# Optimization experiments

Measured on AMD Instinct MI355X. Metric: run time of the kernel, lower is better.

The kernel has to match this reference:

```python
import jax, jax.numpy as jnp
import numpy as np

N = 100000       # num nodes
E = 1600000      # num edges
D_IN = 32
D_HID = 32
D_OUT = 32
K = 3            # Chebyshev order (number of terms)


def setup_inputs() -> dict:
    key = jax.random.key(0)
    k1, k2, k3, k4, k5, k6 = jax.random.split(key, 6)
    x = jax.random.normal(k1, (N, D_IN), dtype=jnp.float32)
    edge_index = jax.random.randint(k2, (2, E), 0, N, dtype=jnp.int64)
    s1 = 1.0 / np.sqrt(D_IN)
    s2 = 1.0 / np.sqrt(D_HID)
    W1 = jax.random.uniform(k3, (K, D_IN, D_HID), jnp.float32, -s1, s1)
    b1 = jax.random.uniform(k4, (D_HID,), jnp.float32, -s1, s1)
    W2 = jax.random.uniform(k5, (K, D_HID, D_OUT), jnp.float32, -s2, s2)
    b2 = jax.random.uniform(k6, (D_OUT,), jnp.float32, -s2, s2)
    return {"x": x, "edge_index": edge_index, "W1": W1, "b1": b1, "W2": W2, "b2": b2}


def _prop(x, row, col, w):
    # L_hat @ x : gather along col, scale by edge weight, scatter-add to row.
    # (diagonal of the rescaled Laplacian cancels to 0 in PyG ChebConv with
    #  sym normalization and lambda_max=2, so only off-diagonal edges remain)
    return jax.ops.segment_sum(w[:, None] * x[col], row, num_segments=N)


def _cheb_conv(x, row, col, w, W, b):
    # Chebyshev recurrence: Tx0 = x, Tx1 = L_hat x, Tx_k = 2 L_hat Tx_{k-1} - Tx_{k-2}
    k_terms = W.shape[0]
    Tx0 = x
    out = Tx0 @ W[0]
    if k_terms > 1:
        Tx1 = _prop(Tx0, row, col, w)
        out = out + Tx1 @ W[1]
        for k in range(2, k_terms):
            Tx2 = 2.0 * _prop(Tx1, row, col, w) - Tx0
            out = out + Tx2 @ W[k]
            Tx0, Tx1 = Tx1, Tx2
    return out + b


def reference(x, edge_index, W1, b1, W2, b2):
    row, col = edge_index[0], edge_index[1]
    mask = (row != col).astype(x.dtype)            # remove_self_loops
    deg = jax.ops.segment_sum(mask, row, num_segments=N)
    dinv = jnp.where(deg > 0, 1.0 / jnp.sqrt(jnp.maximum(deg, 1.0)), 0.0)
    w = -mask * dinv[row] * dinv[col]              # scaled Laplacian off-diagonal weights
    x0 = x
    h = jax.nn.relu(_cheb_conv(x, row, col, w, W1, b1))
    h = _cheb_conv(h, row, col, w, W2, b2)
    return h + x0
```

## Files before the change

kernel.cpp:

```cpp
#include <hip/hip_runtime.h>

#define NN 100000
#define EE 1600000
#define DD 32
#define NBUK 196
#define BROWS 512
#define TILE 4096
#define NT 391
#define BCAP2 10240
#define BSLOT 12288

typedef unsigned int uint;
typedef unsigned short ushort;
typedef unsigned char uchar;
typedef __attribute__((ext_vector_type(8))) short bf16x8;
typedef __attribute__((ext_vector_type(4))) float f32x4;

__device__ __forceinline__ ushort f2b(float f) {
    uint u = __float_as_uint(f);
    u += 0x7fffu + ((u >> 16) & 1u);
    return (ushort)(u >> 16);
}
__device__ __forceinline__ float b2f(ushort h) {
    return __uint_as_float((uint)h << 16);
}
__device__ __forceinline__ uint f2e4(float f) {
    uint u = __float_as_uint(f);
    uint s = (u >> 24) & 0x80u;
    float a = fabsf(f) * 0x1p-120f;
    uint g = __float_as_uint(a);
    g += 0x7FFFFu + ((g >> 20) & 1u);
    uint m = g >> 20;
    if (m > 0x7Eu) m = 0x7Eu;
    return s | m;
}
__device__ __forceinline__ bf16x8 as_bf16x8(uint4 v) {
    union { uint4 u; bf16x8 b; } cv; cv.u = v; return cv.b;
}
__device__ __forceinline__ void acc8(float* acc, uint2 v) {
#pragma unroll
    for (int wi = 0; wi < 2; ++wi) {
        uint w = (&v.x)[wi];
        acc[wi * 4 + 0] += 0x1p120f * __uint_as_float(((w & 0x80u) << 24) | ((w & 0x7fu) << 20));
        acc[wi * 4 + 1] += 0x1p120f * __uint_as_float(((w & 0x8000u) << 16) | ((w & 0x7f00u) << 12));
        acc[wi * 4 + 2] += 0x1p120f * __uint_as_float(((w & 0x800000u) << 8) | ((w & 0x7f0000u) << 4));
        acc[wi * 4 + 3] += 0x1p120f * __uint_as_float((w & 0x80000000u) | ((w & 0x7f000000u) >> 4));
    }
}


__global__ void k_part(const int* __restrict__ ei, int* __restrict__ gtail,
                       int* __restrict__ pairs) {
    __shared__ int hist[256];
    __shared__ int gbase[256];
    int t = threadIdx.x;
    hist[t] = 0;
    __syncthreads();
    int e0 = blockIdx.x * TILE;
    int pk[16], rk[16], bb[16];
#pragma unroll
    for (int k = 0; k < 16; ++k) {
        int e = e0 + t + k * 256;
        bb[k] = -1;
        if (e < EE) {
            int r = ei[e], c = ei[EE + e];
            if (r != c) {
                bb[k] = r >> 9;
                pk[k] = (r & (BROWS - 1)) | (c << 9);
                rk[k] = atomicAdd(&hist[bb[k]], 1);
            }
        }
    }
    __syncthreads();
    if (t < NBUK) {
        int cnt = hist[t];
        gbase[t] = cnt ? atomicAdd(&gtail[t * 16], cnt) : 0;
    }
    __syncthreads();
#pragma unroll
    for (int k = 0; k < 16; ++k) {
        if (bb[k] >= 0) {
            int pos = gbase[bb[k]] + rk[k];
            if (pos < BCAP2) pairs[bb[k] * BCAP2 + pos] = pk[k];
        }
    }
}


__global__ void k_build2(const int* __restrict__ gtail, const int* __restrict__ pairs,
                         float* __restrict__ dinv, int* __restrict__ desc,
                         int* __restrict__ ghist, int* __restrict__ ent) {
    __shared__ int lcnt[BROWS];
    __shared__ int loff[BROWS];
    __shared__ int part[256];
    __shared__ int lh[16];
    __shared__ int slab[BSLOT];
    int b = blockIdx.x, t = threadIdx.x;
    lcnt[t] = 0; lcnt[t + 256] = 0;
    if (t < 16) lh[t] = 0;
    __syncthreads();
    int cnt = gtail[b * 16]; if (cnt > BCAP2) cnt = BCAP2;
    const int* pp = pairs + b * BCAP2;
    for (int i = t; i < cnt; i += 256)
        atomicAdd(&lcnt[pp[i] & (BROWS - 1)], 1);
    __syncthreads();
    int v0 = lcnt[2 * t], v1 = lcnt[2 * t + 1];
    int s0 = v0 > 64 ? 64 : v0; s0 = (s0 + 7) & ~7;
    int s1 = v1 > 64 ? 64 : v1; s1 = (s1 + 7) & ~7;
    part[t] = s0 + s1;
    __syncthreads();
    for (int d = 1; d < 256; d <<= 1) {
        int x = part[t];
        int y = (t >= d) ? part[t - d] : 0;
        __syncthreads();
        part[t] = x + y;
        __syncthreads();
    }
    int excl = (t == 0) ? 0 : part[t - 1];
    loff[2 * t] = excl;
    loff[2 * t + 1] = excl + s0;
    __syncthreads();
    int rowbase = b * BROWS;
    for (int lr = t; lr < BROWS; lr += 256) {
        int n = rowbase + lr;
        if (n < NN) {
            int d = lcnt[lr];
            int ms = d > 64 ? 64 : d;
            int cls = (ms + 7) >> 3;
            dinv[n] = d > 0 ? rsqrtf((float)d) : 0.0f;
            desc[n] = ((b * BSLOT + loff[lr]) >> 3) | (cls << 24);
            atomicAdd(&lh[cls], 1);
        }
    }
    __syncthreads();
    if (t < 16 && lh[t]) atomicAdd(&ghist[t], lh[t]);
    lcnt[t] = 0; lcnt[t + 256] = 0;
    for (int i = t; i < BSLOT; i += 256) slab[i] = NN;
    __syncthreads();
    for (int i = t; i < cnt; i += 256) {
        int v = pp[i];
        int lr = v & (BROWS - 1);
        int pos = atomicAdd(&lcnt[lr], 1);
        if (pos < 64) slab[loff[lr] + pos] = (int)((uint)v >> 9);
    }
    __syncthreads();
    int padded = part[255];
    for (int i = t; i < padded; i += 256)
        ent[(size_t)b * BSLOT + i] = slab[i];
}


__global__ void k_perms(const int* __restrict__ desc, int* __restrict__ classcur,
                        int2* __restrict__ pdesc) {
    __shared__ int h[16];
    __shared__ int base[16];
    if (threadIdx.x < 16) h[threadIdx.x] = 0;
    __syncthreads();
    int n = blockIdx.x * blockDim.x + threadIdx.x;
    int d = 0, cls = 0, rk = 0;
    if (n < NN) {
        d = desc[n];
        cls = (d >> 24) & 15;
        rk = atomicAdd(&h[cls], 1);
    }
    __syncthreads();
    if (threadIdx.x < 16 && h[threadIdx.x])
        base[threadIdx.x] = atomicAdd(&classcur[threadIdx.x], h[threadIdx.x]);
    __syncthreads();
    if (n < NN) {
        int2 v; v.x = n; v.y = d;
        pdesc[base[cls] + rk] = v;
    }
}


__global__ void k_cvt(const float* __restrict__ x, uint2* __restrict__ xb,
                      uint* __restrict__ xb8, const float* __restrict__ dinv,
                      const float* __restrict__ W1, const float* __restrict__ W2,
                      ushort* __restrict__ wb1, ushort* __restrict__ wb2,
                      const int* __restrict__ ghist, int* __restrict__ classcur,
                      uint* __restrict__ t1b8, uint* __restrict__ hb8) {
    if (blockIdx.x == (NN * DD / 4) / 256) {
        for (int i = threadIdx.x; i < 6144; i += 256) {
            const float* W = W1; ushort* wb = wb1;
            int ii = i;
            if (ii >= 3072) { ii -= 3072; W = W2; wb = wb2; }
            int term = ii >> 10, rem = ii & 1023;
            int h = rem >> 9, lane = (rem >> 3) & 63, j = rem & 7;
            int k = ((lane >> 4) << 3) + j;
            int col = (h << 4) | (lane & 15);
            wb[ii] = f2b(W[term * 1024 + k * 32 + col]);
        }
        return;
    }
    if (blockIdx.x == 0) {
        if (threadIdx.x == 0) {
            int s = 0;
            for (int i = 0; i < 16; ++i) { classcur[i] = s; s += ghist[i]; }
        }
        if (threadIdx.x >= 64 && threadIdx.x < 72) xb8[NN * 8 + threadIdx.x - 64] = 0;
        if (threadIdx.x >= 72 && threadIdx.x < 80) t1b8[NN * 8 + threadIdx.x - 72] = 0;
        if (threadIdx.x >= 80 && threadIdx.x < 88) hb8[NN * 8 + threadIdx.x - 80] = 0;
    }
    int tid = blockIdx.x * blockDim.x + threadIdx.x;
    if (tid >= NN * DD / 4) return;
    float4 v = ((const float4*)x)[tid];
    uint2 b;
    b.x = (uint)f2b(v.x) | ((uint)f2b(v.y) << 16);
    b.y = (uint)f2b(v.z) | ((uint)f2b(v.w) << 16);
    xb[tid] = b;
    float dv = dinv[tid >> 3];
    xb8[tid] = f2e4(dv * v.x) | (f2e4(dv * v.y) << 8)
             | (f2e4(dv * v.z) << 16) | (f2e4(dv * v.w) << 24);
}


__global__ void k_prop(const int2* __restrict__ pdesc, const int* __restrict__ ent,
                       const float* __restrict__ dinv,
                       const uint2* __restrict__ src8d,
                       const uint4* __restrict__ baseq,
                       uint2* __restrict__ dst8d,
                       uint4* __restrict__ dstbq,
                       float alpha, float beta) {
    int tid = blockIdx.x * blockDim.x + threadIdx.x;
    int g = tid >> 3;
    if (g >= NN) return;
    int sub = tid & 3, h = (tid >> 2) & 1;
    int2 pd = pdesc[g];
    int n = pd.x;
    const int* ep = ent + ((size_t)(pd.y & 0xFFFFFF) << 3);
    int mr = ((pd.y >> 24) & 15) << 3;
    float acc[8] = {0, 0, 0, 0, 0, 0, 0, 0};
    for (int i = h * 8; i < mr; i += 16) {
        uint4 C0 = *(const uint4*)(ep + i);
        uint4 C1 = *(const uint4*)(ep + i + 4);
        uint2 v0 = src8d[(C0.x << 2) + sub];
        uint2 v1 = src8d[(C0.y << 2) + sub];
        uint2 v2 = src8d[(C0.z << 2) + sub];
        uint2 v3 = src8d[(C0.w << 2) + sub];
        uint2 v4 = src8d[(C1.x << 2) + sub];
        uint2 v5 = src8d[(C1.y << 2) + sub];
        uint2 v6 = src8d[(C1.z << 2) + sub];
        uint2 v7 = src8d[(C1.w << 2) + sub];
        acc8(acc, v0);
        acc8(acc, v1);
        acc8(acc, v2);
        acc8(acc, v3);
        acc8(acc, v4);
        acc8(acc, v5);
        acc8(acc, v6);
        acc8(acc, v7);
    }
    float dn = dinv[n];
    float s = -alpha * dn;
#pragma unroll
    for (int k = 0; k < 8; ++k)
        acc[k] = s * (acc[k] + __shfl_xor(acc[k], 4, 64));
    if (baseq) {
        uint4 b = baseq[(n << 2) + sub];
#pragma unroll
        for (int wi = 0; wi < 4; ++wi) {
            uint w = (&b.x)[wi];
            acc[wi * 2 + 0] += beta * __uint_as_float(w << 16);
            acc[wi * 2 + 1] += beta * __uint_as_float(w & 0xffff0000u);
        }
    }
    if (h == 0) {
        uint4 ob;
#pragma unroll
        for (int wi = 0; wi < 4; ++wi)
            (&ob.x)[wi] = (uint)f2b(acc[wi * 2]) | ((uint)f2b(acc[wi * 2 + 1]) << 16);
        dstbq[(n << 2) + sub] = ob;
    } else if (dst8d) {
        uint2 o8;
        o8.x = f2e4(dn * acc[0]) | (f2e4(dn * acc[1]) << 8)
             | (f2e4(dn * acc[2]) << 16) | (f2e4(dn * acc[3]) << 24);
        o8.y = f2e4(dn * acc[4]) | (f2e4(dn * acc[5]) << 8)
             | (f2e4(dn * acc[6]) << 16) | (f2e4(dn * acc[7]) << 24);
        dst8d[(n << 2) + sub] = o8;
    }
}


__global__ void k_comb(const uint4* __restrict__ t0, const uint4* __restrict__ t1,
                       const uint4* __restrict__ t2, const ushort* __restrict__ wb,
                       const float* __restrict__ bias, const float* __restrict__ residf,
                       const float* __restrict__ dinv,
                       float* __restrict__ outf, ushort* __restrict__ outb,
                       uchar* __restrict__ outb8, int do_relu) {
    int lane = threadIdx.x & 63;
    int wid = threadIdx.x >> 6;
    int n0 = (blockIdx.x * 4 + wid) << 6;
    if (n0 >= NN) return;
    int q = lane >> 4, lr = lane & 15;
    const uint4* wq = (const uint4*)wb;
    bf16x8 bf[3][2];
#pragma unroll
    for (int t = 0; t < 3; ++t)
#pragma unroll
        for (int h = 0; h < 2; ++h)
            bf[t][h] = as_bf16x8(wq[((t * 2 + h) << 6) + lane]);
    float bias0 = bias[lr], bias1 = bias[16 + lr];
    uint4 z; z.x = 0; z.y = 0; z.z = 0; z.w = 0;
#pragma unroll
    for (int mt = 0; mt < 4; ++mt) {
        int nb = n0 + (mt << 4);
        int row = nb + lr;
        bool ok = row < NN;
        int ai = (row << 2) + q;
        bf16x8 a0 = as_bf16x8(ok ? t0[ai] : z);
        bf16x8 a1 = as_bf16x8(ok ? t1[ai] : z);
        bf16x8 a2 = as_bf16x8(ok ? t2[ai] : z);
        f32x4 c0 = {0.f, 0.f, 0.f, 0.f};
        f32x4 c1 = {0.f, 0.f, 0.f, 0.f};
        c0 = __builtin_amdgcn_mfma_f32_16x16x32_bf16(a0, bf[0][0], c0, 0, 0, 0);
        c0 = __builtin_amdgcn_mfma_f32_16x16x32_bf16(a1, bf[1][0], c0, 0, 0, 0);
        c0 = __builtin_amdgcn_mfma_f32_16x16x32_bf16(a2, bf[2][0], c0, 0, 0, 0);
        c1 = __builtin_amdgcn_mfma_f32_16x16x32_bf16(a0, bf[0][1], c1, 0, 0, 0);
        c1 = __builtin_amdgcn_mfma_f32_16x16x32_bf16(a1, bf[1][1], c1, 0, 0, 0);
        c1 = __builtin_amdgcn_mfma_f32_16x16x32_bf16(a2, bf[2][1], c1, 0, 0, 0);
#pragma unroll
        for (int r = 0; r < 4; ++r) {
            int node = nb + (q << 2) + r;
            if (node >= NN) continue;
            float v0 = c0[r] + bias0;
            float v1 = c1[r] + bias1;
            if (do_relu) { v0 = fmaxf(v0, 0.0f); v1 = fmaxf(v1, 0.0f); }
            if (outb) {
                float dv = dinv[node];
                outb[node * DD + lr] = f2b(v0);
                outb[node * DD + 16 + lr] = f2b(v1);
                outb8[node * DD + lr] = (uchar)f2e4(dv * v0);
                outb8[node * DD + 16 + lr] = (uchar)f2e4(dv * v1);
            } else {
                outf[node * DD + lr] = v0 + residf[node * DD + lr];
                outf[node * DD + 16 + lr] = v1 + residf[node * DD + 16 + lr];
            }
        }
    }
}


extern "C" void kernel_launch(void* const* d_in, const int* in_sizes, int n_in,
                              void* d_out, int out_size, void* d_ws, size_t ws_size,
                              hipStream_t stream) {
    const float* x  = (const float*)d_in[0];
    const int*   ei = (const int*)d_in[1];
    const float* W1 = (const float*)d_in[2];
    const float* b1 = (const float*)d_in[3];
    const float* W2 = (const float*)d_in[4];
    const float* b2 = (const float*)d_in[5];
    float* out = (float*)d_out;

    char* wsp = (char*)d_ws;
    size_t off = 0;
    auto take = [&](size_t bytes) {
        char* p = wsp + off;
        off = (off + bytes + 255) & ~(size_t)255;
        return p;
    };
    int*    ctrl  = (int*)take((size_t)(NBUK * 16 + 32) * 4);
    int*    gtail = ctrl;
    int*    ghist = ctrl + NBUK * 16;
    int*    ccur  = ctrl + NBUK * 16 + 16;
    float*  dinv  = (float*)take((size_t)NN * 4);
    int*    desc  = (int*)take((size_t)NN * 4);
    int2*   pdesc = (int2*)take((size_t)NN * 8);
    ushort* wb1   = (ushort*)take((size_t)3072 * 2);
    ushort* wb2   = (ushort*)take((size_t)3072 * 2);
    int*    pairs = (int*)take((size_t)NBUK * BCAP2 * 4);
    int*    ent   = (int*)take((size_t)NBUK * BSLOT * 4);
    ushort* xb    = (ushort*)take((size_t)NN * DD * 2);
    ushort* t1b   = (ushort*)take((size_t)NN * DD * 2);
    ushort* t2b   = (ushort*)take((size_t)NN * DD * 2);
    ushort* hb    = (ushort*)take((size_t)NN * DD * 2);
    uchar*  xb8   = (uchar*)take((size_t)(NN + 1) * DD);
    uchar*  t1b8  = (uchar*)take((size_t)(NN + 1) * DD);
    uchar*  hb8   = (uchar*)take((size_t)(NN + 1) * DD);

    hipMemsetAsync(ctrl, 0, (size_t)(NBUK * 16 + 32) * 4, stream);

    k_part  <<<NT, 256, 0, stream>>>(ei, gtail, pairs);
    k_build2<<<NBUK, 256, 0, stream>>>(gtail, pairs, dinv, desc, ghist, ent);
    k_cvt   <<<NN * DD / 4 / 256 + 1, 256, 0, stream>>>(x, (uint2*)xb, (uint*)xb8, dinv,
                                                        W1, W2, wb1, wb2, ghist, ccur,
                                                        (uint*)t1b8, (uint*)hb8);
    k_perms <<<(NN + 255) / 256, 256, 0, stream>>>(desc, ccur, pdesc);

    const int pgrid = (NN * 8 + 255) / 256;
    const int mgrid = (NN + 255) / 256;
    k_prop<<<pgrid, 256, 0, stream>>>(pdesc, ent, dinv, (const uint2*)xb8, nullptr,
                                      (uint2*)t1b8, (uint4*)t1b, 1.0f, 0.0f);
    k_prop<<<pgrid, 256, 0, stream>>>(pdesc, ent, dinv, (const uint2*)t1b8,
                                      (const uint4*)xb, nullptr, (uint4*)t2b, 2.0f, -1.0f);
    k_comb<<<mgrid, 256, 0, stream>>>((const uint4*)xb, (const uint4*)t1b,
                                      (const uint4*)t2b, wb1, b1, nullptr, dinv,
                                      nullptr, hb, hb8, 1);
    k_prop<<<pgrid, 256, 0, stream>>>(pdesc, ent, dinv, (const uint2*)hb8, nullptr,
                                      (uint2*)t1b8, (uint4*)t1b, 1.0f, 0.0f);
    k_prop<<<pgrid, 256, 0, stream>>>(pdesc, ent, dinv, (const uint2*)t1b8,
                                      (const uint4*)hb, nullptr, (uint4*)t2b, 2.0f, -1.0f);
    k_comb<<<mgrid, 256, 0, stream>>>((const uint4*)hb, (const uint4*)t1b,
                                      (const uint4*)t2b, wb2, b2, x, dinv,
                                      out, nullptr, nullptr, 0);
}
```

Baseline: 255.4 us.

## Halve bucket size, fold class prefix into build and perms into convert kernel

Buckets now cover 256 rows instead of 512, giving 391 smaller buckets so the build kernel runs more blocks with one row per thread and less shared memory. The class-offset prefix sum moves into the last-finishing build block, found with a done counter and threadfence. The permutation kernel is merged into the convert kernel as extra blocks, removing one launch. This relies on last-block detection being correct, and smaller bucket capacities raise the risk of overflow and silently dropped edges.

```diff
diff --git a/kernel.cpp b/kernel.cpp
--- a/kernel.cpp
+++ b/kernel.cpp
@@ -3,12 +3,13 @@
 #define NN 100000
 #define EE 1600000
 #define DD 32
-#define NBUK 196
-#define BROWS 512
+#define NBUK 391
+#define BROWS 256
 #define TILE 4096
 #define NT 391
-#define BCAP2 10240
-#define BSLOT 12288
+#define BCAP2 4864
+#define BSLOT 5888
+#define CVB 3125
 
 typedef unsigned int uint;
 typedef unsigned short ushort;
@@ -51,10 +52,10 @@
 
 __global__ void k_part(const int* __restrict__ ei, int* __restrict__ gtail,
                        int* __restrict__ pairs) {
-    __shared__ int hist[256];
-    __shared__ int gbase[256];
+    __shared__ int hist[512];
+    __shared__ int gbase[512];
     int t = threadIdx.x;
-    hist[t] = 0;
+    hist[t] = 0; hist[t + 256] = 0;
     __syncthreads();
     int e0 = blockIdx.x * TILE;
     int pk[16], rk[16], bb[16];
@@ -65,16 +66,16 @@
         if (e < EE) {
             int r = ei[e], c = ei[EE + e];
             if (r != c) {
-                bb[k] = r >> 9;
-                pk[k] = (r & (BROWS - 1)) | (c << 9);
+                bb[k] = r >> 8;
+                pk[k] = (r & (BROWS - 1)) | (c << 8);
                 rk[k] = atomicAdd(&hist[bb[k]], 1);
             }
         }
     }
     __syncthreads();
-    if (t < NBUK) {
-        int cnt = hist[t];
-        gbase[t] = cnt ? atomicAdd(&gtail[t * 16], cnt) : 0;
+    for (int q = t; q < NBUK; q += 256) {
+        int cnt = hist[q];
+        gbase[q] = cnt ? atomicAdd(&gtail[q * 16], cnt) : 0;
     }
     __syncthreads();
 #pragma unroll
@@ -89,14 +90,16 @@
 
 __global__ void k_build2(const int* __restrict__ gtail, const int* __restrict__ pairs,
                          float* __restrict__ dinv, int* __restrict__ desc,
-                         int* __restrict__ ghist, int* __restrict__ ent) {
+                         int* __restrict__ ghist, int* __restrict__ ent,
+                         int* __restrict__ done, int* __restrict__ classcur) {
     __shared__ int lcnt[BROWS];
     __shared__ int loff[BROWS];
     __shared__ int part[256];
     __shared__ int lh[16];
     __shared__ int slab[BSLOT];
+    __shared__ int isLast;
     int b = blockIdx.x, t = threadIdx.x;
-    lcnt[t] = 0; lcnt[t + 256] = 0;
+    lcnt[t] = 0;
     if (t < 16) lh[t] = 0;
     __syncthreads();
     int cnt = gtail[b * 16]; if (cnt > BCAP2) cnt = BCAP2;
@@ -104,10 +107,9 @@
     for (int i = t; i < cnt; i += 256)
         atomicAdd(&lcnt[pp[i] & (BROWS - 1)], 1);
     __syncthreads();
-    int v0 = lcnt[2 * t], v1 = lcnt[2 * t + 1];
+    int v0 = lcnt[t];
     int s0 = v0 > 64 ? 64 : v0; s0 = (s0 + 7) & ~7;
-    int s1 = v1 > 64 ? 64 : v1; s1 = (s1 + 7) & ~7;
-    part[t] = s0 + s1;
+    part[t] = s0;
     __syncthreads();
     for (int d = 1; d < 256; d <<= 1) {
         int x = part[t];
@@ -116,60 +118,42 @@
         part[t] = x + y;
         __syncthreads();
     }
-    int excl = (t == 0) ? 0 : part[t - 1];
-    loff[2 * t] = excl;
-    loff[2 * t + 1] = excl + s0;
-    __syncthreads();
-    int rowbase = b * BROWS;
-    for (int lr = t; lr < BROWS; lr += 256) {
-        int n = rowbase + lr;
-        if (n < NN) {
-            int d = lcnt[lr];
-            int ms = d > 64 ? 64 : d;
-            int cls = (ms + 7) >> 3;
-            dinv[n] = d > 0 ? rsqrtf((float)d) : 0.0f;
-            desc[n] = ((b * BSLOT + loff[lr]) >> 3) | (cls << 24);
-            atomicAdd(&lh[cls], 1);
-        }
+    int excl = part[t] - s0;
+    loff[t] = excl;
+    int n = b * BROWS + t;
+    if (n < NN) {
+        int d = v0;
+        int ms = d > 64 ? 64 : d;
+        int cls = (ms + 7) >> 3;
+        dinv[n] = d > 0 ? rsqrtf((float)d) : 0.0f;
+        desc[n] = ((b * BSLOT + excl) >> 3) | (cls << 24);
+        atomicAdd(&lh[cls], 1);
     }
     __syncthreads();
     if (t < 16 && lh[t]) atomicAdd(&ghist[t], lh[t]);
-    lcnt[t] = 0; lcnt[t + 256] = 0;
+    lcnt[t] = 0;
     for (int i = t; i < BSLOT; i += 256) slab[i] = NN;
     __syncthreads();
     for (int i = t; i < cnt; i += 256) {
         int v = pp[i];
         int lr = v & (BROWS - 1);
         int pos = atomicAdd(&lcnt[lr], 1);
-        if (pos < 64) slab[loff[lr] + pos] = (int)((uint)v >> 9);
+        if (pos < 64) slab[loff[lr] + pos] = (int)((uint)v >> 8);
     }
     __syncthreads();
     int padded = part[255];
     for (int i = t; i < padded; i += 256)
         ent[(size_t)b * BSLOT + i] = slab[i];
-}
-
-
-__global__ void k_perms(const int* __restrict__ desc, int* __restrict__ classcur,
-                        int2* __restrict__ pdesc) {
-    __shared__ int h[16];
-    __shared__ int base[16];
-    if (threadIdx.x < 16) h[threadIdx.x] = 0;
-    __syncthreads();
-    int n = blockIdx.x * blockDim.x + threadIdx.x;
-    int d = 0, cls = 0, rk = 0;
-    if (n < NN) {
-        d = desc[n];
-        cls = (d >> 24) & 15;
-        rk = atomicAdd(&h[cls], 1);
-    }
-    __syncthreads();
-    if (threadIdx.x < 16 && h[threadIdx.x])
-        base[threadIdx.x] = atomicAdd(&classcur[threadIdx.x], h[threadIdx.x]);
-    __syncthreads();
-    if (n < NN) {
-        int2 v; v.x = n; v.y = d;
-        pdesc[base[cls] + rk] = v;
+    __threadfence();
+    if (t == 0) isLast = (atomicAdd(done, 1) == NBUK - 1);
+    __syncthreads();
+    if (isLast && t == 0) {
+        __threadfence();
+        int s = 0;
+        for (int i = 0; i < 16; ++i) {
+            int g = atomicAdd(&ghist[i], 0);
+            classcur[i] = s; s += g;
+        }
     }
 }
 
@@ -178,9 +162,10 @@
                       uint* __restrict__ xb8, const float* __restrict__ dinv,
                       const float* __restrict__ W1, const float* __restrict__ W2,
                       ushort* __restrict__ wb1, ushort* __restrict__ wb2,
-                      const int* __restrict__ ghist, int* __restrict__ classcur,
+                      const int* __restrict__ desc, int* __restrict__ classcur,
+                      int2* __restrict__ pdesc,
                       uint* __restrict__ t1b8, uint* __restrict__ hb8) {
-    if (blockIdx.x == (NN * DD / 4) / 256) {
+    if (blockIdx.x == CVB) {
         for (int i = threadIdx.x; i < 6144; i += 256) {
             const float* W = W1; ushort* wb = wb1;
             int ii = i;
@@ -193,11 +178,29 @@
         }
         return;
     }
+    if (blockIdx.x > CVB) {
+        __shared__ int h[16];
+        __shared__ int base[16];
+        if (threadIdx.x < 16) h[threadIdx.x] = 0;
+        __syncthreads();
+        int n = (blockIdx.x - CVB - 1) * 256 + threadIdx.x;
+        int d = 0, cls = 0, rk = 0;
+        if (n < NN) {
+            d = desc[n];
+            cls = (d >> 24) & 15;
+            rk = atomicAdd(&h[cls], 1);
+        }
+        __syncthreads();
+        if (threadIdx.x < 16 && h[threadIdx.x])
+            base[threadIdx.x] = atomicAdd(&classcur[threadIdx.x], h[threadIdx.x]);
+        __syncthreads();
+        if (n < NN) {
+            int2 v; v.x = n; v.y = d;
+            pdesc[base[cls] + rk] = v;
+        }
+        return;
+    }
     if (blockIdx.x == 0) {
-        if (threadIdx.x == 0) {
-            int s = 0;
-            for (int i = 0; i < 16; ++i) { classcur[i] = s; s += ghist[i]; }
-        }
         if (threadIdx.x >= 64 && threadIdx.x < 72) xb8[NN * 8 + threadIdx.x - 64] = 0;
         if (threadIdx.x >= 72 && threadIdx.x < 80) t1b8[NN * 8 + threadIdx.x - 72] = 0;
         if (threadIdx.x >= 80 && threadIdx.x < 88) hb8[NN * 8 + threadIdx.x - 80] = 0;
@@ -359,10 +362,11 @@
         off = (off + bytes + 255) & ~(size_t)255;
         return p;
     };
-    int*    ctrl  = (int*)take((size_t)(NBUK * 16 + 32) * 4);
+    int*    ctrl  = (int*)take((size_t)(NBUK * 16 + 48) * 4);
     int*    gtail = ctrl;
     int*    ghist = ctrl + NBUK * 16;
     int*    ccur  = ctrl + NBUK * 16 + 16;
+    int*    done  = ctrl + NBUK * 16 + 32;
     float*  dinv  = (float*)take((size_t)NN * 4);
     int*    desc  = (int*)take((size_t)NN * 4);
     int2*   pdesc = (int2*)take((size_t)NN * 8);
@@ -378,14 +382,13 @@
     uchar*  t1b8  = (uchar*)take((size_t)(NN + 1) * DD);
     uchar*  hb8   = (uchar*)take((size_t)(NN + 1) * DD);
 
-    hipMemsetAsync(ctrl, 0, (size_t)(NBUK * 16 + 32) * 4, stream);
+    hipMemsetAsync(ctrl, 0, (size_t)(NBUK * 16 + 48) * 4, stream);
 
     k_part  <<<NT, 256, 0, stream>>>(ei, gtail, pairs);
-    k_build2<<<NBUK, 256, 0, stream>>>(gtail, pairs, dinv, desc, ghist, ent);
-    k_cvt   <<<NN * DD / 4 / 256 + 1, 256, 0, stream>>>(x, (uint2*)xb, (uint*)xb8, dinv,
-                                                        W1, W2, wb1, wb2, ghist, ccur,
-                                                        (uint*)t1b8, (uint*)hb8);
-    k_perms <<<(NN + 255) / 256, 256, 0, stream>>>(desc, ccur, pdesc);
+    k_build2<<<NBUK, 256, 0, stream>>>(gtail, pairs, dinv, desc, ghist, ent, done, ccur);
+    k_cvt   <<<CVB + 1 + (NN + 255) / 256, 256, 0, stream>>>(
+                x, (uint2*)xb, (uint*)xb8, dinv, W1, W2, wb1, wb2,
+                desc, ccur, pdesc, (uint*)t1b8, (uint*)hb8);
 
     const int pgrid = (NN * 8 + 255) / 256;
     const int mgrid = (NN + 255) / 256;
```

New measurement: 286.4 us. 12.2% more time.

## Use fixed 64-slot per-row adjacency layout with smaller buckets in graph build

Applied to the files above, without the earlier changes.

Shrinks row buckets from 512 to 128 rows (782 buckets) and replaces the prefix-sum-packed adjacency slab with a fixed 64 entries per row, so each row's offset is simply n*64. This drops the counting pass, the block-wide scan and its many barriers from the build kernel, and raises its block count. In exchange the adjacency array grows and is written in full (padding included), and the partition kernel now keeps larger shared histograms and does more global atomics per block.

```diff
diff --git a/kernel.cpp b/kernel.cpp
--- a/kernel.cpp
+++ b/kernel.cpp
@@ -3,12 +3,11 @@
 #define NN 100000
 #define EE 1600000
 #define DD 32
-#define NBUK 196
-#define BROWS 512
+#define NBUK 782
+#define BROWS 128
 #define TILE 4096
 #define NT 391
-#define BCAP2 10240
-#define BSLOT 12288
+#define BCAP2 2560
 
 typedef unsigned int uint;
 typedef unsigned short ushort;
@@ -51,10 +50,10 @@
 
 __global__ void k_part(const int* __restrict__ ei, int* __restrict__ gtail,
                        int* __restrict__ pairs) {
-    __shared__ int hist[256];
-    __shared__ int gbase[256];
+    __shared__ int hist[NBUK];
+    __shared__ int gbase[NBUK];
     int t = threadIdx.x;
-    hist[t] = 0;
+    for (int q = t; q < NBUK; q += 256) hist[q] = 0;
     __syncthreads();
     int e0 = blockIdx.x * TILE;
     int pk[16], rk[16], bb[16];
@@ -65,16 +64,16 @@
         if (e < EE) {
             int r = ei[e], c = ei[EE + e];
             if (r != c) {
-                bb[k] = r >> 9;
-                pk[k] = (r & (BROWS - 1)) | (c << 9);
+                bb[k] = r >> 7;
+                pk[k] = (r & (BROWS - 1)) | (c << 7);
                 rk[k] = atomicAdd(&hist[bb[k]], 1);
             }
         }
     }
     __syncthreads();
-    if (t < NBUK) {
-        int cnt = hist[t];
-        gbase[t] = cnt ? atomicAdd(&gtail[t * 16], cnt) : 0;
+    for (int q = t; q < NBUK; q += 256) {
+        int cnt = hist[q];
+        gbase[q] = cnt ? atomicAdd(&gtail[q * 16], cnt) : 0;
     }
     __syncthreads();
 #pragma unroll
@@ -91,62 +90,38 @@
                          float* __restrict__ dinv, int* __restrict__ desc,
                          int* __restrict__ ghist, int* __restrict__ ent) {
     __shared__ int lcnt[BROWS];
-    __shared__ int loff[BROWS];
-    __shared__ int part[256];
     __shared__ int lh[16];
-    __shared__ int slab[BSLOT];
+    __shared__ int slab[BROWS * 64];
     int b = blockIdx.x, t = threadIdx.x;
-    lcnt[t] = 0; lcnt[t + 256] = 0;
+    if (t < BROWS) lcnt[t] = 0;
     if (t < 16) lh[t] = 0;
+    for (int i = t; i < BROWS * 64; i += 256) slab[i] = NN;
     __syncthreads();
     int cnt = gtail[b * 16]; if (cnt > BCAP2) cnt = BCAP2;
     const int* pp = pairs + b * BCAP2;
-    for (int i = t; i < cnt; i += 256)
-        atomicAdd(&lcnt[pp[i] & (BROWS - 1)], 1);
-    __syncthreads();
-    int v0 = lcnt[2 * t], v1 = lcnt[2 * t + 1];
-    int s0 = v0 > 64 ? 64 : v0; s0 = (s0 + 7) & ~7;
-    int s1 = v1 > 64 ? 64 : v1; s1 = (s1 + 7) & ~7;
-    part[t] = s0 + s1;
-    __syncthreads();
-    for (int d = 1; d < 256; d <<= 1) {
-        int x = part[t];
-        int y = (t >= d) ? part[t - d] : 0;
-        __syncthreads();
-        part[t] = x + y;
-        __syncthreads();
-    }
-    int excl = (t == 0) ? 0 : part[t - 1];
-    loff[2 * t] = excl;
-    loff[2 * t + 1] = excl + s0;
-    __syncthreads();
-    int rowbase = b * BROWS;
-    for (int lr = t; lr < BROWS; lr += 256) {
-        int n = rowbase + lr;
-        if (n < NN) {
-            int d = lcnt[lr];
-            int ms = d > 64 ? 64 : d;
-            int cls = (ms + 7) >> 3;
-            dinv[n] = d > 0 ? rsqrtf((float)d) : 0.0f;
-            desc[n] = ((b * BSLOT + loff[lr]) >> 3) | (cls << 24);
-            atomicAdd(&lh[cls], 1);
-        }
-    }
-    __syncthreads();
-    if (t < 16 && lh[t]) atomicAdd(&ghist[t], lh[t]);
-    lcnt[t] = 0; lcnt[t + 256] = 0;
-    for (int i = t; i < BSLOT; i += 256) slab[i] = NN;
-    __syncthreads();
     for (int i = t; i < cnt; i += 256) {
         int v = pp[i];
         int lr = v & (BROWS - 1);
         int pos = atomicAdd(&lcnt[lr], 1);
-        if (pos < 64) slab[loff[lr] + pos] = (int)((uint)v >> 9);
-    }
-    __syncthreads();
-    int padded = part[255];
-    for (int i = t; i < padded; i += 256)
-        ent[(size_t)b * BSLOT + i] = slab[i];
+        if (pos < 64) slab[(lr << 6) + pos] = (int)((uint)v >> 7);
+    }
+    __syncthreads();
+    if (t < BROWS) {
+        int n = b * BROWS + t;
+        if (n < NN) {
+            int d = lcnt[t];
+            int ms = d > 64 ? 64 : d;
+            int cls = (ms + 7) >> 3;
+            dinv[n] = d > 0 ? rsqrtf((float)d) : 0.0f;
+            desc[n] = (n << 3) | (cls << 24);
+            atomicAdd(&lh[cls], 1);
+        }
+    }
+    __syncthreads();
+    if (t < 16 && lh[t]) atomicAdd(&ghist[t], lh[t]);
+    int base = b * (BROWS * 64);
+    for (int i = t; i < BROWS * 64; i += 256)
+        ent[base + i] = slab[i];
 }
 
 
@@ -369,7 +344,7 @@
     ushort* wb1   = (ushort*)take((size_t)3072 * 2);
     ushort* wb2   = (ushort*)take((size_t)3072 * 2);
     int*    pairs = (int*)take((size_t)NBUK * BCAP2 * 4);
-    int*    ent   = (int*)take((size_t)NBUK * BSLOT * 4);
+    int*    ent   = (int*)take((size_t)NBUK * BROWS * 64 * 4);
     ushort* xb    = (ushort*)take((size_t)NN * DD * 2);
     ushort* t1b   = (ushort*)take((size_t)NN * DD * 2);
     ushort* t2b   = (ushort*)take((size_t)NN * DD * 2);
```

After: 262.0 us. +2.6%, slower.
